# Optimization experiments

Hardware: AMD Instinct MI355X
Metric: run time of the kernel (lower is better)

The kernel has to match this reference:

```python
import jax, jax.numpy as jnp
import numpy as np

# Water box constants: n_atoms=192 -> 64 oxygens (type 8) + 128 hydrogens (type 1)
N_O, N_H = 64, 128
XLIM = 6.0  # params.max_rdf_dist


def _hist(d, bins):
    """np.histogram-equivalent fixed-bin histogram of 1-D values d."""
    nb = bins.shape[0] - 1
    idx = jnp.clip(jnp.searchsorted(bins, d, side='right') - 1, 0, nb - 1)
    w = ((d >= bins[0]) & (d <= bins[-1])).astype(jnp.float32)
    return jnp.zeros((nb,), jnp.float32).at[idx].add(w)


def _pair_rdf(wrapped, idx0, idx1, lattices, bins):
    # wrapped: [T, N, 3]; replicates distance_pbc_select + histogram/RDF math
    x0 = wrapped[:, idx0]                       # [T, n0, 3] (type1 atoms)
    x1 = wrapped[:, idx1]                       # [T, n1, 3] (type2 atoms)
    # x0.repeat([1,n1,1]) vs x1.repeat_interleave(n0) == outer pairing (x1 outer, x0 inner)
    delta = jnp.abs(x0[:, None, :, :] - x1[:, :, None, :])   # [T, n1, n0, 3]
    delta = jnp.where(delta > 0.5 * lattices, delta - lattices, delta)
    s = (delta ** 2).sum(-1)                    # [T, n1, n0]
    # safe sqrt (self-pairs give exact zeros)
    d = jnp.where(s > 0, jnp.sqrt(jnp.where(s > 0, s, 1.0)), 0.0)
    T = d.shape[0]
    P = d.shape[1] * d.shape[2]
    d = d.reshape(T, P)
    hists = jax.vmap(lambda dd: _hist(dd, bins))(d)          # [T, nb]
    vol = jnp.prod(lattices)
    shell = (4.0 / 3.0) * jnp.pi * (bins[1:] ** 3 - bins[:-1] ** 3)
    # aggregate RDF over all frames (zeros fall below bins[0]=1e-6, excluded)
    Z1 = (T * P / vol) * shell
    data_rdf = hists.sum(0) / Z1
    # per-frame RDFs, renormalized to the aggregate RDF's total mass
    Z2 = (T / vol) * shell
    rdfs = hists / Z2
    rdfs = rdfs / rdfs.sum(1, keepdims=True) * data_rdf.sum()
    return rdfs.mean(0)                          # [nb]


def setup_inputs() -> dict:
    key = jax.random.key(0)
    k0, k1, k2, k3 = jax.random.split(key, 4)
    T, R, N, nb = 100, 8, 192, 600
    stacked_radii = jax.random.normal(k0, (T, R, N, 3), jnp.float32) * 5.0
    ptypes = jnp.tile(jnp.array([8, 1, 1], jnp.int32), N // 3)  # O,H,H per water
    lattices = jnp.full((3,), 12.42, jnp.float32)
    bins = jnp.asarray(np.linspace(1e-6, XLIM, nb + 1), jnp.float32)
    gt_oo = jax.random.uniform(k1, (1, nb), jnp.float32)
    gt_hh = jax.random.uniform(k2, (1, nb), jnp.float32)
    gt_ho = jax.random.uniform(k3, (1, nb), jnp.float32)
    return dict(stacked_radii=stacked_radii, ptypes=ptypes, lattices=lattices,
                bins=bins, gt_oo=gt_oo, gt_hh=gt_hh, gt_ho=gt_ho)


def reference(stacked_radii, ptypes, lattices, bins, gt_oo, gt_hh, gt_ho):
    idx_O = jnp.nonzero(ptypes == 8, size=N_O)[0]
    idx_H = jnp.nonzero(ptypes == 1, size=N_H)[0]

    def per_replica(data):                       # data: [T, N, 3]
        wrapped = data / lattices % 1 * lattices  # PBC wrap into box
        rdf_oo = _pair_rdf(wrapped, idx_O, idx_O, lattices, bins)
        rdf_hh = _pair_rdf(wrapped, idx_H, idx_H, lattices, bins)
        rdf_ho = _pair_rdf(wrapped, idx_H, idx_O, lattices, bins)
        maes = jnp.stack([
            XLIM * jnp.abs(rdf_oo[None] - gt_oo).mean(),
            XLIM * jnp.abs(rdf_hh[None] - gt_hh).mean(),
            XLIM * jnp.abs(rdf_ho[None] - gt_ho).mean(),
        ])
        return jnp.concatenate([rdf_oo, rdf_hh, rdf_ho]), maes.max()

    # [T, R, N, 3] -> [R, T, N, 3], vmap over replicas
    rdf_list, max_maes = jax.vmap(per_replica)(jnp.swapaxes(stacked_radii, 0, 1))
    return rdf_list, max_maes
```

## Files before the change

### kernel.cpp

```cpp
#include <hip/hip_runtime.h>

#define T_STEPS 100
#define R_REP   8
#define N_ATOMS 192
#define NBINS   600

__global__ __launch_bounds__(256) void rdf_hist_kernel(
    const float* __restrict__ radii,
    const float* __restrict__ lattices,
    const float* __restrict__ bins,
    float* __restrict__ hist_out,
    float* __restrict__ sigma_out)
{
#pragma clang fp contract(off)
    __shared__ float    Tq[NBINS + 2];
    __shared__ unsigned shist[2][3][NBINS];
    __shared__ float4   sAtom[192];
    __shared__ float    spart[4][3];

    const int blk = blockIdx.x;
    const int t   = blk % T_STEPS;
    const int r   = blk / T_STEPS;
    const int tid = threadIdx.x;

    for (int b = tid; b <= NBINS + 1; b += 256) {
        if (b <= NBINS) {
            float e = bins[b];
            unsigned u = __float_as_uint(e * e);
            while (sqrtf(__uint_as_float(u)) <  e) ++u;
            while (sqrtf(__uint_as_float(u - 1)) >= e) --u;
            Tq[b] = __uint_as_float(u);
        } else {
            unsigned u = __float_as_uint(36.0f);
            while (sqrtf(__uint_as_float(u)) <= 6.0f) ++u;
            while (sqrtf(__uint_as_float(u - 1)) > 6.0f) --u;
            Tq[NBINS + 1] = __uint_as_float(u);
        }
    }
    for (int b = tid; b < NBINS; b += 256) {
        shist[0][0][b] = 0u; shist[0][1][b] = 0u; shist[0][2][b] = 0u;
        shist[1][0][b] = 0u; shist[1][1][b] = 0u; shist[1][2][b] = 0u;
    }

    const float L0 = lattices[0], L1 = lattices[1], L2 = lattices[2];
    const float* base = radii + (size_t)(t * R_REP + r) * (N_ATOMS * 3);

    for (int a = tid; a < 192; a += 256) {
        int atom = (a < 64) ? (3 * a)
                            : (3 * ((a - 64) >> 1) + 1 + ((a - 64) & 1));
        const float* src = base + atom * 3;
        float x = src[0], y = src[1], z = src[2];
        float qx = x / L0; float wx = (qx - floorf(qx)) * L0;
        float qy = y / L1; float wy = (qy - floorf(qy)) * L1;
        float qz = z / L2; float wz = (qz - floorf(qz)) * L2;
        sAtom[a] = make_float4(wx, wy, wz, 0.0f);
    }
    __syncthreads();

    const float T0 = Tq[0];
    const float TG = Tq[NBINS + 1];
    const float b0f = bins[0];
    const float invstep = (float)NBINS / (6.0f - b0f);
    const int bank = tid >> 7;

    auto bin_pair = [&](const float4& A, const float4& B, unsigned w,
                        unsigned* myh) {
#pragma clang fp contract(off)
        float dx = fabsf(A.x - B.x); dx = fminf(dx, fabsf(dx - L0));
        float dy = fabsf(A.y - B.y); dy = fminf(dy, fabsf(dy - L1));
        float dz = fabsf(A.z - B.z); dz = fminf(dz, fabsf(dz - L2));
        float s = dx * dx + dy * dy + dz * dz;
        if (s < T0 || s >= TG) return;
        float dhat = __builtin_amdgcn_sqrtf(s);
        int k0 = (int)((dhat - b0f) * invstep);
        if (k0 > NBINS - 1) k0 = NBINS - 1;
        float lo = Tq[k0], hi = Tq[k0 + 1];
        int bi = k0 + (int)(s >= hi) - (int)(s < lo);
        if (bi > NBINS - 1) bi = NBINS - 1;
        atomicAdd(&myh[bi], w);
    };

    {
        int i = tid & 63;
        float4 A = sAtom[i];
        int kbase = (tid >> 6) + 1;
        unsigned* myh = shist[bank][0];
#pragma unroll
        for (int it = 0; it < 8; ++it) {
            int k = kbase + it * 4;
            bin_pair(A, sAtom[(i + k) & 63], (k == 32) ? 1u : 2u, myh);
        }
    }
    {
        int i = tid & 127;
        float4 A = sAtom[64 + i];
        int kbase = (tid >> 7) + 1;
        unsigned* myh = shist[bank][1];
#pragma unroll
        for (int it = 0; it < 32; ++it) {
            int k = kbase + it * 2;
            bin_pair(A, sAtom[64 + ((i + k) & 127)], (k == 64) ? 1u : 2u, myh);
        }
    }
    {
        int i = tid & 127;
        float4 A = sAtom[64 + i];
        int jbase = tid >> 7;
        unsigned* myh = shist[bank][2];
#pragma unroll
        for (int it = 0; it < 32; ++it)
            bin_pair(A, sAtom[jbase + it * 2], 1u, myh);
    }
    __syncthreads();

    float lsig0 = 0.0f, lsig1 = 0.0f, lsig2 = 0.0f;
    float* outp = hist_out + ((size_t)(r * 3) * T_STEPS + t) * NBINS;
    for (int b = tid; b < NBINS; b += 256) {
        float e0 = bins[b], e1 = bins[b + 1];
        float shell = 4.18879020478639053f * (e1 * e1 * e1 - e0 * e0 * e0);
        float f0 = (float)(shist[0][0][b] + shist[1][0][b]);
        float f1 = (float)(shist[0][1][b] + shist[1][1][b]);
        float f2 = (float)(shist[0][2][b] + shist[1][2][b]);
        outp[b] = f0;
        outp[(size_t)T_STEPS * NBINS + b] = f1;
        outp[(size_t)(2 * T_STEPS) * NBINS + b] = f2;
        lsig0 += f0 / shell;
        lsig1 += f1 / shell;
        lsig2 += f2 / shell;
    }
    for (int off = 32; off > 0; off >>= 1) {
        lsig0 += __shfl_down(lsig0, off);
        lsig1 += __shfl_down(lsig1, off);
        lsig2 += __shfl_down(lsig2, off);
    }
    const int wid = tid >> 6, lane = tid & 63;
    if (lane == 0) {
        spart[wid][0] = lsig0; spart[wid][1] = lsig1; spart[wid][2] = lsig2;
    }
    __syncthreads();
    if (tid < 3) {
        float s = spart[0][tid] + spart[1][tid] + spart[2][tid] + spart[3][tid];
        sigma_out[(r * 3 + tid) * T_STEPS + t] = s;
    }
}

__global__ __launch_bounds__(640) void rdf_norm_kernel(
    const float* __restrict__ hist,
    const float* __restrict__ sigma,
    const float* __restrict__ bins,
    const float* __restrict__ lattices,
    const float* __restrict__ gt_oo,
    const float* __restrict__ gt_hh,
    const float* __restrict__ gt_ho,
    float* __restrict__ out)
{
#pragma clang fp contract(off)
    __shared__ float ssig[T_STEPS];
    __shared__ float sinvsig[T_STEPS];
    __shared__ float swred[10];
    __shared__ float sS;

    const int blk = blockIdx.x;
    const int p = blk % 3, r = blk / 3;
    const int tid = threadIdx.x;
    const float* h = hist + (size_t)blk * T_STEPS * NBINS;

    if (tid < T_STEPS) {
        float sg = sigma[blk * T_STEPS + tid];
        ssig[tid] = sg;
        sinvsig[tid] = 1.0f / sg;
    }
    __syncthreads();
    if (tid == 0) {
        float s = 0.0f;
        for (int t = 0; t < T_STEPS; ++t) s += ssig[t];
        float vol = lattices[0] * lattices[1] * lattices[2];
        float Pf = (p == 0) ? 4096.0f : ((p == 1) ? 16384.0f : 8192.0f);
        sS = vol / ((float)T_STEPS * Pf) * s;
    }
    __syncthreads();

    const float S = sS;
    const float* gt = (p == 0) ? gt_oo : ((p == 1) ? gt_hh : gt_ho);
    float lacc = 0.0f;
    const int b = tid;
    if (b < NBINS) {
        float a0 = 0.0f, a1 = 0.0f, a2 = 0.0f, a3 = 0.0f;
        const float* hb = h + b;
        for (int t = 0; t < T_STEPS; t += 4) {
            a0 += hb[(t + 0) * NBINS] * sinvsig[t + 0];
            a1 += hb[(t + 1) * NBINS] * sinvsig[t + 1];
            a2 += hb[(t + 2) * NBINS] * sinvsig[t + 2];
            a3 += hb[(t + 3) * NBINS] * sinvsig[t + 3];
        }
        float e0 = bins[b], e1 = bins[b + 1];
        float shell = 4.18879020478639053f * (e1 * e1 * e1 - e0 * e0 * e0);
        float v = S * (1.0f / (float)T_STEPS) * (1.0f / shell) * ((a0 + a1) + (a2 + a3));
        out[r * 1800 + p * 600 + b] = v;
        lacc = fabsf(v - gt[b]);
    }
    for (int off = 32; off > 0; off >>= 1)
        lacc += __shfl_down(lacc, off);
    const int wid = tid >> 6, lane = tid & 63;
    if (lane == 0) swred[wid] = lacc;
    __syncthreads();
    if (tid == 0) {
        float s = 0.0f;
        for (int w = 0; w < 10; ++w) s += swred[w];
        float mae = 6.0f * (s / 600.0f);
        atomicMax((int*)&out[14400 + r], __float_as_int(mae));
    }
}

extern "C" void kernel_launch(void* const* d_in, const int* in_sizes, int n_in,
                              void* d_out, int out_size, void* d_ws, size_t ws_size,
                              hipStream_t stream) {
    const float* radii    = (const float*)d_in[0];
    const float* lattices = (const float*)d_in[2];
    const float* bins     = (const float*)d_in[3];
    const float* gt_oo    = (const float*)d_in[4];
    const float* gt_hh    = (const float*)d_in[5];
    const float* gt_ho    = (const float*)d_in[6];
    float* out = (float*)d_out;

    float* hist  = (float*)d_ws;
    float* sigma = hist + (size_t)R_REP * 3 * T_STEPS * NBINS;

    hipLaunchKernelGGL(rdf_hist_kernel, dim3(R_REP * T_STEPS), dim3(256), 0, stream,
                       radii, lattices, bins, hist, sigma);
    hipLaunchKernelGGL(rdf_norm_kernel, dim3(R_REP * 3), dim3(640), 0, stream,
                       hist, sigma, bins, lattices, gt_oo, gt_hh, gt_ho, out);
}
```

Before: 92.88 us.

## Rebalance pair work across waves with per-wave histogram copies

The pair loops are re-partitioned so every wave takes an equal share of the OO, HH and HO pairs, and each thread handles two anchor atoms. Histograms are replicated per wave (4 copies instead of 2) to cut LDS atomic contention, and they are zeroed with 16-byte stores. The norm kernel's time loop gets 8 accumulators for more memory-level parallelism. This costs more LDS (about 28 KB of histograms) and a 4-way reduction at the end, and the reordered floating-point accumulation in the norm kernel can change rounding slightly.

```diff
diff --git a/kernel.cpp b/kernel.cpp
--- a/kernel.cpp
+++ b/kernel.cpp
@@ -14,7 +14,7 @@
 {
 #pragma clang fp contract(off)
     __shared__ float    Tq[NBINS + 2];
-    __shared__ unsigned shist[2][3][NBINS];
+    __shared__ __align__(16) unsigned shist[4][3][NBINS];
     __shared__ float4   sAtom[192];
     __shared__ float    spart[4][3];
 
@@ -37,9 +37,10 @@
             Tq[NBINS + 1] = __uint_as_float(u);
         }
     }
-    for (int b = tid; b < NBINS; b += 256) {
-        shist[0][0][b] = 0u; shist[0][1][b] = 0u; shist[0][2][b] = 0u;
-        shist[1][0][b] = 0u; shist[1][1][b] = 0u; shist[1][2][b] = 0u;
+    {
+        uint4* z = (uint4*)&shist[0][0][0];
+        const uint4 z4 = make_uint4(0u, 0u, 0u, 0u);
+        for (int idx = tid; idx < (4 * 3 * NBINS) / 4; idx += 256) z[idx] = z4;
     }
 
     const float L0 = lattices[0], L1 = lattices[1], L2 = lattices[2];
@@ -61,7 +62,10 @@
     const float TG = Tq[NBINS + 1];
     const float b0f = bins[0];
     const float invstep = (float)NBINS / (6.0f - b0f);
-    const int bank = tid >> 7;
+    const int wid = tid >> 6;
+    unsigned* h_oo = shist[wid][0];
+    unsigned* h_hh = shist[wid][1];
+    unsigned* h_ho = shist[wid][2];
 
     auto bin_pair = [&](const float4& A, const float4& B, unsigned w,
                         unsigned* myh) {
@@ -81,35 +85,51 @@
     };
 
     {
+        int i = tid & 31;
+        float4 Aa = sAtom[i];
+        float4 Ab = sAtom[32 + i];
+        int kb = tid >> 5;
+#pragma unroll
+        for (int it = 0; it < 2; ++it) {
+            int k = kb + 1 + it * 8;
+            unsigned w = (k == 16) ? 1u : 2u;
+            int jj = (i + k) & 31;
+            bin_pair(Aa, sAtom[jj], w, h_oo);
+            bin_pair(Ab, sAtom[32 + jj], w, h_oo);
+        }
+#pragma unroll
+        for (int it = 0; it < 4; ++it) {
+            int j = kb + it * 8;
+            bin_pair(Aa, sAtom[32 + j], 2u, h_oo);
+        }
+    }
+    {
         int i = tid & 63;
-        float4 A = sAtom[i];
-        int kbase = (tid >> 6) + 1;
-        unsigned* myh = shist[bank][0];
+        float4 A0 = sAtom[64 + i];
+        float4 A1 = sAtom[128 + i];
+        int kb = (tid >> 6) + 1;
 #pragma unroll
         for (int it = 0; it < 8; ++it) {
-            int k = kbase + it * 4;
-            bin_pair(A, sAtom[(i + k) & 63], (k == 32) ? 1u : 2u, myh);
+            int k = kb + it * 4;
+            unsigned w = (k == 32) ? 1u : 2u;
+            int jj = (i + k) & 63;
+            bin_pair(A0, sAtom[64 + jj], w, h_hh);
+            bin_pair(A1, sAtom[128 + jj], w, h_hh);
+        }
+        int jb = tid >> 6;
+#pragma unroll
+        for (int it = 0; it < 16; ++it) {
+            int j = jb + it * 4;
+            bin_pair(A0, sAtom[128 + j], 2u, h_hh);
         }
     }
     {
         int i = tid & 127;
         float4 A = sAtom[64 + i];
-        int kbase = (tid >> 7) + 1;
-        unsigned* myh = shist[bank][1];
-#pragma unroll
-        for (int it = 0; it < 32; ++it) {
-            int k = kbase + it * 2;
-            bin_pair(A, sAtom[64 + ((i + k) & 127)], (k == 64) ? 1u : 2u, myh);
-        }
-    }
-    {
-        int i = tid & 127;
-        float4 A = sAtom[64 + i];
-        int jbase = tid >> 7;
-        unsigned* myh = shist[bank][2];
+        int jb = tid >> 7;
 #pragma unroll
         for (int it = 0; it < 32; ++it)
-            bin_pair(A, sAtom[jbase + it * 2], 1u, myh);
+            bin_pair(A, sAtom[jb + it * 2], 1u, h_ho);
     }
     __syncthreads();
 
@@ -118,9 +138,9 @@
     for (int b = tid; b < NBINS; b += 256) {
         float e0 = bins[b], e1 = bins[b + 1];
         float shell = 4.18879020478639053f * (e1 * e1 * e1 - e0 * e0 * e0);
-        float f0 = (float)(shist[0][0][b] + shist[1][0][b]);
-        float f1 = (float)(shist[0][1][b] + shist[1][1][b]);
-        float f2 = (float)(shist[0][2][b] + shist[1][2][b]);
+        float f0 = (float)(shist[0][0][b] + shist[1][0][b] + shist[2][0][b] + shist[3][0][b]);
+        float f1 = (float)(shist[0][1][b] + shist[1][1][b] + shist[2][1][b] + shist[3][1][b]);
+        float f2 = (float)(shist[0][2][b] + shist[1][2][b] + shist[2][2][b] + shist[3][2][b]);
         outp[b] = f0;
         outp[(size_t)T_STEPS * NBINS + b] = f1;
         outp[(size_t)(2 * T_STEPS) * NBINS + b] = f2;
@@ -133,7 +153,7 @@
         lsig1 += __shfl_down(lsig1, off);
         lsig2 += __shfl_down(lsig2, off);
     }
-    const int wid = tid >> 6, lane = tid & 63;
+    const int lane = tid & 63;
     if (lane == 0) {
         spart[wid][0] = lsig0; spart[wid][1] = lsig1; spart[wid][2] = lsig2;
     }
@@ -186,16 +206,26 @@
     const int b = tid;
     if (b < NBINS) {
         float a0 = 0.0f, a1 = 0.0f, a2 = 0.0f, a3 = 0.0f;
+        float a4 = 0.0f, a5 = 0.0f, a6 = 0.0f, a7 = 0.0f;
         const float* hb = h + b;
-        for (int t = 0; t < T_STEPS; t += 4) {
+        for (int t = 0; t < 96; t += 8) {
             a0 += hb[(t + 0) * NBINS] * sinvsig[t + 0];
             a1 += hb[(t + 1) * NBINS] * sinvsig[t + 1];
             a2 += hb[(t + 2) * NBINS] * sinvsig[t + 2];
             a3 += hb[(t + 3) * NBINS] * sinvsig[t + 3];
-        }
+            a4 += hb[(t + 4) * NBINS] * sinvsig[t + 4];
+            a5 += hb[(t + 5) * NBINS] * sinvsig[t + 5];
+            a6 += hb[(t + 6) * NBINS] * sinvsig[t + 6];
+            a7 += hb[(t + 7) * NBINS] * sinvsig[t + 7];
+        }
+        a0 += hb[96 * NBINS] * sinvsig[96];
+        a1 += hb[97 * NBINS] * sinvsig[97];
+        a2 += hb[98 * NBINS] * sinvsig[98];
+        a3 += hb[99 * NBINS] * sinvsig[99];
+        float asum = ((a0 + a1) + (a2 + a3)) + ((a4 + a5) + (a6 + a7));
         float e0 = bins[b], e1 = bins[b + 1];
         float shell = 4.18879020478639053f * (e1 * e1 * e1 - e0 * e0 * e0);
-        float v = S * (1.0f / (float)T_STEPS) * (1.0f / shell) * ((a0 + a1) + (a2 + a3));
+        float v = S * (1.0f / (float)T_STEPS) * (1.0f / shell) * asum;
         out[r * 1800 + p * 600 + b] = v;
         lacc = fabsf(v - gt[b]);
     }
```

Measured after the change: 92.43 us. No clear change (-0.5%).
